# Kernel tuning notes

Measured on AMD Instinct MI355X. Metric: run time of the kernel, lower is better.

## Reference

```python
import jax, jax.numpy as jnp
import numpy as np

D_MODEL = 1024
N_HEADS = 16
D_FF = 4096
EPS = 1e-5


def setup_inputs() -> dict:
    key = jax.random.key(0)
    ks = jax.random.split(key, 10)
    sig_attn = (1.0 / D_MODEL) ** 0.5
    sig1 = (2.0 / (D_MODEL + D_FF)) ** 0.5
    sig2 = (2.0 / (D_FF + D_MODEL)) ** 0.5
    return {
        "x": jax.random.normal(ks[0], (4, 2048, D_MODEL), dtype=jnp.float32),
        "W_q": jax.random.normal(ks[1], (D_MODEL, D_MODEL), jnp.float32) * sig_attn,
        "W_k": jax.random.normal(ks[2], (D_MODEL, D_MODEL), jnp.float32) * sig_attn,
        "W_v": jax.random.normal(ks[3], (D_MODEL, D_MODEL), jnp.float32) * sig_attn,
        "W_o": jax.random.normal(ks[4], (D_MODEL, D_MODEL), jnp.float32) * sig_attn,
        "gamma1": jnp.ones((D_MODEL,), jnp.float32),
        "gamma2": jnp.ones((D_MODEL,), jnp.float32),
        "W1": jax.random.normal(ks[5], (D_FF, D_MODEL), jnp.float32) * sig1,  # gate proj
        "W2": jax.random.normal(ks[6], (D_MODEL, D_FF), jnp.float32) * sig2,  # down proj
        "W3": jax.random.normal(ks[7], (D_FF, D_MODEL), jnp.float32) * sig1,  # up proj
    }


def _rmsnorm(x, gamma, eps=EPS):
    # computed in fp32 as in the original, cast back to input dtype
    in_dtype = x.dtype
    xf = x.astype(jnp.float32)
    norm = jnp.sqrt(jnp.mean(xf * xf, axis=-1, keepdims=True) + eps)
    return ((xf / norm) * gamma).astype(in_dtype)


def _mha(x, W_q, W_k, W_v, W_o, n_heads=N_HEADS):
    B, S, D = x.shape
    d_h = D // n_heads
    # projections: weights stored as [d_out, d_in]
    q = jnp.einsum('bsd,ed->bse', x, W_q).reshape(B, S, n_heads, d_h).transpose(0, 2, 1, 3)
    k = jnp.einsum('bsd,ed->bse', x, W_k).reshape(B, S, n_heads, d_h).transpose(0, 2, 1, 3)
    v = jnp.einsum('bsd,ed->bse', x, W_v).reshape(B, S, n_heads, d_h).transpose(0, 2, 1, 3)
    scores = jnp.einsum('bhqd,bhkd->bhqk', q, k) / jnp.sqrt(jnp.asarray(d_h, x.dtype))
    causal = jnp.tril(jnp.ones((S, S), dtype=bool))  # True = keep
    scores = jnp.where(causal, scores, -jnp.inf)
    probs = jax.nn.softmax(scores, axis=-1)
    out = jnp.einsum('bhqk,bhkd->bhqd', probs, v)
    out = out.transpose(0, 2, 1, 3).reshape(B, S, D)
    return jnp.einsum('bse,de->bsd', out, W_o)


def _swiglu(x, W1, W2, W3):
    g = jnp.einsum('bsd,fd->bsf', x, W1)
    u = jnp.einsum('bsd,fd->bsf', x, W3)
    return jnp.einsum('bsf,df->bsd', jax.nn.silu(g) * u, W2)


def reference(x, W_q, W_k, W_v, W_o, gamma1, gamma2, W1, W2, W3):
    x = x + _mha(_rmsnorm(x, gamma1), W_q, W_k, W_v, W_o)
    x = x + _swiglu(_rmsnorm(x, gamma2), W1, W2, W3)
    return x
```

## Files before the change

kernel.cpp:

```cpp
#include <hip/hip_runtime.h>
#include <cstdint>
#include <cstddef>

typedef unsigned short u16;
typedef unsigned int u32;
typedef short bf16x8 __attribute__((ext_vector_type(8)));
typedef float f32x4 __attribute__((ext_vector_type(4)));
typedef float f32x16 __attribute__((ext_vector_type(16)));
typedef u16 u16x4 __attribute__((ext_vector_type(4)));

__device__ __forceinline__ u16 f2bf(float f) {
  u32 u = __float_as_uint(f);
  return (u16)((u + 0x7FFFu + ((u >> 16) & 1u)) >> 16);
}
__device__ __forceinline__ float bf2f(u16 h) {
  return __uint_as_float(((u32)h) << 16);
}
__device__ __forceinline__ u32 cvtpk(float lo, float hi) {
  u32 r;
  asm("v_cvt_pk_bf16_f32 %0, %1, %2" : "=v"(r) : "v"(lo), "v"(hi));
  return r;
}
__device__ __forceinline__ float exp2a(float x) {
  float r;
  asm("v_exp_f32 %0, %1" : "=v"(r) : "v"(x));
  return r;
}

__device__ __forceinline__ void gload_lds16(const void* g, void* l) {
  __builtin_amdgcn_global_load_lds((const __attribute__((address_space(1))) u32*)g,
                                   (__attribute__((address_space(3))) u32*)l, 16, 0, 0);
}

__global__ __launch_bounds__(256) void castw(const float* __restrict__ src,
                                             u16* __restrict__ dst, int n4) {
  int i = blockIdx.x * 256 + threadIdx.x;
  if (i < n4) {
    float4 v = ((const float4*)src)[i];
    u16x4 r;
    r.x = f2bf(v.x); r.y = f2bf(v.y); r.z = f2bf(v.z); r.w = f2bf(v.w);
    ((u16x4*)dst)[i] = r;
  }
}

__global__ __launch_bounds__(256) void rmsnorm_k(const float* __restrict__ x,
                                                 const float* __restrict__ gamma,
                                                 u16* __restrict__ o) {
  const int row = blockIdx.x;
  const int t = threadIdx.x;
  float4 v = ((const float4*)(x + (size_t)row * 1024))[t];
  float ss = v.x * v.x + v.y * v.y + v.z * v.z + v.w * v.w;
  #pragma unroll
  for (int m = 1; m < 64; m <<= 1) ss += __shfl_xor(ss, m);
  __shared__ float wsum[4];
  if ((t & 63) == 0) wsum[t >> 6] = ss;
  __syncthreads();
  float tot = wsum[0] + wsum[1] + wsum[2] + wsum[3];
  float inv = rsqrtf(tot * (1.0f / 1024.0f) + 1e-5f);
  float4 g = ((const float4*)gamma)[t];
  u16x4 r;
  r.x = f2bf(v.x * inv * g.x);
  r.y = f2bf(v.y * inv * g.y);
  r.z = f2bf(v.z * inv * g.z);
  r.w = f2bf(v.w * inv * g.w);
  ((u16x4*)(o + (size_t)row * 1024))[t] = r;
}

template <int EPI>
__global__ __launch_bounds__(256, 4)
void gemm128(const u16* __restrict__ A, const u16* __restrict__ B,
             void* out, const void* ep, int M, int N, int KLOOP, int KS,
             float scale, int ncut) {
  __shared__ u16 smem[2][8192];
  u16* const sA = smem[0];
  u16* const sB = smem[1];

  const int tid = threadIdx.x;
  const int lane = tid & 63;
  const int w = tid >> 6;
  const int wr = w >> 1, wc = w & 1;
  const int lr = lane & 15, lk = lane >> 4;

  A += (size_t)blockIdx.z * KLOOP;
  B += (size_t)blockIdx.z * KLOOP;

  const int nx = gridDim.x;
  const int nwg = nx * gridDim.y;
  const int flat = blockIdx.y * nx + blockIdx.x;
  const int qq = nwg >> 3, rr = nwg & 7;
  const int xcd = flat & 7, off = flat >> 3;
  const int swz = (xcd < rr ? xcd * (qq + 1) : rr * (qq + 1) + (xcd - rr) * qq) + off;
  const int sr = nx * 8;
  const int g8 = swz / sr, rem = swz % sr;
  const int m0 = (g8 * 8 + (rem & 7)) * 128;
  const int n0 = (rem >> 3) * 128;

  f32x4 acc[4][4];
  #pragma unroll
  for (int i = 0; i < 4; i++)
    #pragma unroll
    for (int j = 0; j < 4; j++) acc[i][j] = (f32x4){0.f, 0.f, 0.f, 0.f};

  for (int kt = 0; kt < KLOOP; kt += 64) {
    __syncthreads();
    #pragma unroll
    for (int r = 0; r < 4; r++) {
      const int q = r * 256 + tid;
      const int row = q >> 3;
      const int cs = (q & 7) ^ (row & 7);
      gload_lds16(A + (size_t)(m0 + row) * KS + kt + cs * 8, (char*)sA + q * 16);
      gload_lds16(B + (size_t)(n0 + row) * KS + kt + cs * 8, (char*)sB + q * 16);
    }
    __syncthreads();
    #pragma unroll
    for (int kk = 0; kk < 2; kk++) {
      bf16x8 a_[4], b_[4];
      #pragma unroll
      for (int i = 0; i < 4; i++)
        a_[i] = *(const bf16x8*)&sA[(wr * 64 + i * 16 + lr) * 64 +
                                    (((kk * 4 + lk) ^ (lr & 7)) * 8)];
      #pragma unroll
      for (int j = 0; j < 4; j++)
        b_[j] = *(const bf16x8*)&sB[(wc * 64 + j * 16 + lr) * 64 +
                                    (((kk * 4 + lk) ^ (lr & 7)) * 8)];
      #pragma unroll
      for (int i = 0; i < 4; i++)
        #pragma unroll
        for (int j = 0; j < 4; j++)
          acc[i][j] = __builtin_amdgcn_mfma_f32_16x16x32_bf16(a_[i], b_[j], acc[i][j], 0, 0, 0);
    }
  }

  if constexpr (EPI == 1 || EPI == 3) {
    #pragma unroll
    for (int i = 0; i < 4; i++)
      #pragma unroll
      for (int j = 0; j < 4; j++)
        #pragma unroll
        for (int r = 0; r < 4; r++) {
          const int grow = m0 + wr * 64 + i * 16 + lk * 4 + r;
          const int gcol = n0 + wc * 64 + j * 16 + lr;
          const size_t idx = (size_t)grow * N + gcol;
          if (EPI == 1) ((float*)out)[idx] = ((const float*)ep)[idx] + acc[i][j][r];
          else          unsafeAtomicAdd((float*)out + idx, acc[i][j][r]);
        }
  } else {
    u16* const smC = smem[0];
    const float s = (EPI == 0 && n0 < ncut) ? scale : 1.0f;
    __syncthreads();
    #pragma unroll
    for (int i = 0; i < 4; i++)
      #pragma unroll
      for (int j = 0; j < 4; j++)
        #pragma unroll
        for (int r = 0; r < 4; r++) {
          const int row = wr * 64 + i * 16 + lk * 4 + r;
          const int col = wc * 64 + j * 16 + lr;
          smC[row * 128 + (col ^ ((row & 7) << 3))] = f2bf(acc[i][j][r] * s);
        }
    __syncthreads();
    #pragma unroll
    for (int it = 0; it < 8; it++) {
      const int fl = it * 256 + tid;
      const int row = fl >> 4;
      const int ch = fl & 15;
      bf16x8 cv = *(const bf16x8*)&smC[row * 128 + ((ch ^ (row & 7)) * 8)];
      const size_t gidx = (size_t)(m0 + row) * N + n0 + ch * 8;
      if (EPI == 0) {
        *(bf16x8*)((u16*)out + gidx) = cv;
      } else {
        bf16x8 gv = *(const bf16x8*)((const u16*)ep + gidx);
        bf16x8 ov;
        #pragma unroll
        for (int k = 0; k < 8; k++) {
          float g = bf2f((u16)gv[k]);
          float sg = g / (1.f + __expf(-g));
          ov[k] = (short)f2bf(sg * bf2f((u16)cv[k]));
        }
        *(bf16x8*)((u16*)out + gidx) = ov;
      }
    }
  }
}

__global__ __launch_bounds__(256) void vtrans(const u16* __restrict__ qkv,
                                              u16* __restrict__ vt) {
  __shared__ u16 T[64][72];
  const int t = threadIdx.x;
  const int s0 = blockIdx.x * 64;
  const int h = blockIdx.y;
  const int b = blockIdx.z;
  const int sl = t >> 2, dl = (t & 3) * 16;
  const u16* src = qkv + ((size_t)(b * 2048 + s0 + sl)) * 3072 + 2048 + h * 64 + dl;
  bf16x8 v0 = *(const bf16x8*)src;
  bf16x8 v1 = *(const bf16x8*)(src + 8);
  #pragma unroll
  for (int j = 0; j < 8; j++) T[dl + j][sl] = (u16)v0[j];
  #pragma unroll
  for (int j = 0; j < 8; j++) T[dl + 8 + j][sl] = (u16)v1[j];
  __syncthreads();
  const int dl2 = t >> 2, sl2 = (t & 3) * 16;
  u16* dst = vt + ((size_t)((b * 16 + h) * 64 + dl2)) * 2048 + s0 + sl2;
  *(bf16x8*)dst = *(const bf16x8*)&T[dl2][sl2];
  *(bf16x8*)(dst + 8) = *(const bf16x8*)&T[dl2][sl2 + 8];
}

__global__ __launch_bounds__(256, 2)
void attn_fwd3(const u16* __restrict__ qkv, const u16* __restrict__ vt,
               u16* __restrict__ o) {
  __shared__ u16 sm[9216];
  u16* const smK = sm;
  u16* const smV = sm + 4096;

  const int tid = threadIdx.x;
  const int lane = tid & 63;
  const int w = tid >> 6;
  const int hi = lane >> 5;
  const int ln = lane & 31;

  const int bh = blockIdx.x;
  const int pair = blockIdx.y;
  const int b = bh >> 4, h = bh & 15;

  #pragma unroll 1
  for (int phase = 0; phase < 2; ++phase) {
    const int qt = phase ? (15 - pair) : pair;
    const int qbase = qt * 128;
    const int qw0 = qbase + w * 32;
    const int qglob = qw0 + ln;
    const int nkb = qt * 2 + 2;

    bf16x8 qf[4];
    {
      const u16* qp = qkv + ((size_t)(b * 2048 + qw0 + ln)) * 3072 + h * 64 + hi * 8;
      #pragma unroll
      for (int c = 0; c < 4; c++) qf[c] = *(const bf16x8*)(qp + c * 16);
    }

    f32x16 accO[2];
    #pragma unroll
    for (int i = 0; i < 2; i++)
      #pragma unroll
      for (int r = 0; r < 16; r++) accO[i][r] = 0.f;
    float mrun = -1e30f, lsum = 0.f;

    for (int kb = 0; kb < nkb; kb++) {
      const int kbase = kb * 64;
      __syncthreads();
      #pragma unroll
      for (int r = 0; r < 2; r++) {
        const int cb = w * 128 + r * 64;
        const int ci = cb + lane;
        {
          const int key = ci >> 3, gch = (ci & 7) ^ (key & 7);
          const u16* src = qkv + ((size_t)(b * 2048 + kbase + key)) * 3072 + 1024 + h * 64 + gch * 8;
          gload_lds16(src, (char*)smK + cb * 16);
        }
        {
          const int d = ci >> 3, gch = (ci & 7) ^ (d & 7);
          const u16* src = vt + ((size_t)(bh * 64 + d)) * 2048 + kbase + gch * 8;
          gload_lds16(src, (char*)smV + cb * 16);
        }
      }
      __syncthreads();

      if (kbase <= qw0 + 31) {
        f32x16 st[2];
        #pragma unroll
        for (int kt = 0; kt < 2; kt++) {
          #pragma unroll
          for (int r = 0; r < 16; r++) st[kt][r] = 0.f;
        }
        __builtin_amdgcn_s_setprio(1);
        #pragma unroll
        for (int kt = 0; kt < 2; kt++)
          #pragma unroll
          for (int c = 0; c < 4; c++) {
            const int row = kt * 32 + ln;
            const int sch = (c * 2 + hi) ^ (ln & 7);
            bf16x8 kf = *(const bf16x8*)((const char*)smK + row * 128 + sch * 16);
            st[kt] = __builtin_amdgcn_mfma_f32_32x32x16_bf16(kf, qf[c], st[kt], 0, 0, 0);
          }
        __builtin_amdgcn_s_setprio(0);
        if (kbase + 63 > qw0) {
          #pragma unroll
          for (int kt = 0; kt < 2; kt++)
            #pragma unroll
            for (int r = 0; r < 16; r++) {
              const int kk = kbase + kt * 32 + (r & 3) + 8 * (r >> 2) + 4 * hi;
              if (kk > qglob) st[kt][r] = -1e30f;
            }
        }
        float t16[16];
        #pragma unroll
        for (int i = 0; i < 16; i++) t16[i] = fmaxf(st[0][i], st[1][i]);
        #pragma unroll
        for (int s = 8; s > 0; s >>= 1)
          #pragma unroll
          for (int i = 0; i < 8; i++)
            if (i < s) t16[i] = fmaxf(t16[i], t16[i + s]);
        float pm = t16[0];
        pm = fmaxf(pm, __shfl_xor(pm, 32));
        if (!__all(pm - mrun <= 8.f)) {
          const float mnew = fmaxf(mrun, pm);
          const float alpha = exp2a(mrun - mnew);
          lsum *= alpha;
          accO[0] *= alpha;
          accO[1] *= alpha;
          mrun = mnew;
        }
        #pragma unroll
        for (int kt = 0; kt < 2; kt++)
          #pragma unroll
          for (int r = 0; r < 16; r++) st[kt][r] = exp2a(st[kt][r] - mrun);
        float s16[16];
        #pragma unroll
        for (int i = 0; i < 16; i++) s16[i] = st[0][i] + st[1][i];
        #pragma unroll
        for (int s = 8; s > 0; s >>= 1)
          #pragma unroll
          for (int i = 0; i < 8; i++)
            if (i < s) s16[i] = s16[i] + s16[i + s];
        float ps = s16[0];
        ps += __shfl_xor(ps, 32);
        lsum += ps;

        #pragma unroll
        for (int kt = 0; kt < 2; kt++) {
          u32 pw[8], px[8];
          #pragma unroll
          for (int i = 0; i < 8; i++) pw[i] = cvtpk(st[kt][2 * i], st[kt][2 * i + 1]);
          #pragma unroll
          for (int i = 0; i < 8; i++) px[i] = (u32)__shfl_xor((int)pw[i], 32);
          union { u32 wd[4]; bf16x8 v; } f0, f1;
          f0.wd[0] = hi ? px[2] : pw[0];
          f0.wd[1] = hi ? px[3] : pw[1];
          f0.wd[2] = hi ? pw[2] : px[0];
          f0.wd[3] = hi ? pw[3] : px[1];
          f1.wd[0] = hi ? px[6] : pw[4];
          f1.wd[1] = hi ? px[7] : pw[5];
          f1.wd[2] = hi ? pw[6] : px[4];
          f1.wd[3] = hi ? pw[7] : px[5];
          __builtin_amdgcn_s_setprio(1);
          #pragma unroll
          for (int d0 = 0; d0 < 2; d0++) {
            #pragma unroll
            for (int kc = 0; kc < 2; kc++) {
              const int drow = d0 * 32 + ln;
              const int sch = (kt * 4 + kc * 2 + hi) ^ (ln & 7);
              bf16x8 vf = *(const bf16x8*)((const char*)smV + drow * 128 + sch * 16);
              accO[d0] = __builtin_amdgcn_mfma_f32_32x32x16_bf16(vf, kc ? f1.v : f0.v,
                                                                 accO[d0], 0, 0, 0);
            }
          }
          __builtin_amdgcn_s_setprio(0);
        }
      }
    }

    __syncthreads();
    const float inv = 1.0f / lsum;
    #pragma unroll
    for (int d0 = 0; d0 < 2; d0++)
      #pragma unroll
      for (int r = 0; r < 16; r++) {
        const int d = d0 * 32 + (r & 3) + 8 * (r >> 2) + 4 * hi;
        sm[(w * 32 + ln) * 72 + d] = f2bf(accO[d0][r] * inv);
      }
    __syncthreads();
    const int ql = tid >> 1, dh = (tid & 1) * 32;
    const u16* srcp = &sm[ql * 72 + dh];
    u16* dst = o + ((size_t)(b * 2048 + qbase + ql)) * 1024 + h * 64 + dh;
    #pragma unroll
    for (int j = 0; j < 4; j++)
      *(bf16x8*)(dst + j * 8) = *(const bf16x8*)(srcp + j * 8);
    __syncthreads();
  }
}

extern "C" void kernel_launch(void* const* d_in, const int* in_sizes, int n_in,
                              void* d_out, int out_size, void* d_ws, size_t ws_size,
                              hipStream_t stream) {
  const float* x      = (const float*)d_in[0];
  const float* W_q    = (const float*)d_in[1];
  const float* W_k    = (const float*)d_in[2];
  const float* W_v    = (const float*)d_in[3];
  const float* W_o    = (const float*)d_in[4];
  const float* gamma1 = (const float*)d_in[5];
  const float* gamma2 = (const float*)d_in[6];
  const float* W1     = (const float*)d_in[7];
  const float* W2     = (const float*)d_in[8];
  const float* W3     = (const float*)d_in[9];

  char* ws = (char*)d_ws;
  const size_t MB = 1ull << 20;
  u16* qkvw  = (u16*)(ws + 0 * MB);
  u16* Wo_b  = (u16*)(ws + 6 * MB);
  u16* W1_b  = (u16*)(ws + 8 * MB);
  u16* W3_b  = (u16*)(ws + 16 * MB);
  u16* W2_b  = (u16*)(ws + 24 * MB);
  u16* xn    = (u16*)(ws + 32 * MB);
  u16* qkvb  = (u16*)(ws + 48 * MB);
  u16* attnb = (u16*)(ws + 96 * MB);
  u16* vtb   = (u16*)(ws + 112 * MB);
  u16* gbuf  = (u16*)(ws + 112 * MB);
  u16* hbuf  = (u16*)(ws + 48 * MB);
  float* x1  = (float*)d_out;

  castw<<<1024, 256, 0, stream>>>(W_q, qkvw, 262144);
  castw<<<1024, 256, 0, stream>>>(W_k, qkvw + 1024 * 1024, 262144);
  castw<<<1024, 256, 0, stream>>>(W_v, qkvw + 2048 * 1024, 262144);
  castw<<<1024, 256, 0, stream>>>(W_o, Wo_b, 262144);
  castw<<<4096, 256, 0, stream>>>(W1, W1_b, 1048576);
  castw<<<4096, 256, 0, stream>>>(W3, W3_b, 1048576);
  castw<<<4096, 256, 0, stream>>>(W2, W2_b, 1048576);

  rmsnorm_k<<<8192, 256, 0, stream>>>(x, gamma1, xn);
  gemm128<0><<<dim3(24, 64), 256, 0, stream>>>(xn, qkvw, qkvb, nullptr,
                                               8192, 3072, 1024, 1024,
                                               0.125f * 1.44269504f, 1024);
  vtrans<<<dim3(32, 16, 4), 256, 0, stream>>>(qkvb, vtb);
  attn_fwd3<<<dim3(64, 8), 256, 0, stream>>>(qkvb, vtb, attnb);
  gemm128<1><<<dim3(8, 64), 256, 0, stream>>>(attnb, Wo_b, x1, x,
                                              8192, 1024, 1024, 1024, 1.0f, 0);

  rmsnorm_k<<<8192, 256, 0, stream>>>(x1, gamma2, xn);
  gemm128<0><<<dim3(32, 64), 256, 0, stream>>>(xn, W1_b, gbuf, nullptr,
                                               8192, 4096, 1024, 1024, 1.0f, 0);
  gemm128<2><<<dim3(32, 64), 256, 0, stream>>>(xn, W3_b, hbuf, gbuf,
                                               8192, 4096, 1024, 1024, 1.0f, 0);
  gemm128<3><<<dim3(8, 64, 2), 256, 0, stream>>>(hbuf, W2_b, (float*)d_out, nullptr,
                                                 8192, 1024, 2048, 4096, 1.0f, 0);
}
```

Baseline: 489.5 us.

## Double-buffer LDS staging in attention and the W1 gate GEMM

Adds a double-buffered GEMM variant that prefetches the next K tile into a second LDS buffer while computing on the current one, with an XCD-aware workgroup swizzle. It is used only for the W1 gate projection. The attention kernel is also converted to double-buffered K/V staging, so each key block needs one barrier instead of two. The cost is twice the LDS per block, which is meant to hide global-to-LDS latency but lowers occupancy (launch bounds drop to 2 blocks per SM for the GEMM).

```diff
diff --git a/kernel.cpp b/kernel.cpp
--- a/kernel.cpp
+++ b/kernel.cpp
@@ -66,6 +66,7 @@
   ((u16x4*)(o + (size_t)row * 1024))[t] = r;
 }
 
+
 template <int EPI>
 __global__ __launch_bounds__(256, 4)
 void gemm128(const u16* __restrict__ A, const u16* __restrict__ B,
@@ -148,6 +149,131 @@
     u16* const smC = smem[0];
     const float s = (EPI == 0 && n0 < ncut) ? scale : 1.0f;
     __syncthreads();
+    #pragma unroll
+    for (int i = 0; i < 4; i++)
+      #pragma unroll
+      for (int j = 0; j < 4; j++)
+        #pragma unroll
+        for (int r = 0; r < 4; r++) {
+          const int row = wr * 64 + i * 16 + lk * 4 + r;
+          const int col = wc * 64 + j * 16 + lr;
+          smC[row * 128 + (col ^ ((row & 7) << 3))] = f2bf(acc[i][j][r] * s);
+        }
+    __syncthreads();
+    #pragma unroll
+    for (int it = 0; it < 8; it++) {
+      const int fl = it * 256 + tid;
+      const int row = fl >> 4;
+      const int ch = fl & 15;
+      bf16x8 cv = *(const bf16x8*)&smC[row * 128 + ((ch ^ (row & 7)) * 8)];
+      const size_t gidx = (size_t)(m0 + row) * N + n0 + ch * 8;
+      if (EPI == 0) {
+        *(bf16x8*)((u16*)out + gidx) = cv;
+      } else {
+        bf16x8 gv = *(const bf16x8*)((const u16*)ep + gidx);
+        bf16x8 ov;
+        #pragma unroll
+        for (int k = 0; k < 8; k++) {
+          float g = bf2f((u16)gv[k]);
+          float sg = g / (1.f + __expf(-g));
+          ov[k] = (short)f2bf(sg * bf2f((u16)cv[k]));
+        }
+        *(bf16x8*)((u16*)out + gidx) = ov;
+      }
+    }
+  }
+}
+
+template <int EPI>
+__global__ __launch_bounds__(256, 2)
+void gemm128db(const u16* __restrict__ A, const u16* __restrict__ B,
+               void* out, const void* ep, int M, int N, int KLOOP, int KS,
+               float scale, int ncut) {
+  __shared__ u16 sA[2][8192];
+  __shared__ u16 sB[2][8192];
+
+  const int tid = threadIdx.x;
+  const int lane = tid & 63;
+  const int w = tid >> 6;
+  const int wr = w >> 1, wc = w & 1;
+  const int lr = lane & 15, lk = lane >> 4;
+
+  A += (size_t)blockIdx.z * KLOOP;
+  B += (size_t)blockIdx.z * KLOOP;
+
+  const int nx = gridDim.x;
+  const int nwg = nx * gridDim.y;
+  const int flat = blockIdx.y * nx + blockIdx.x;
+  const int qq = nwg >> 3, rr = nwg & 7;
+  const int xcd = flat & 7, off = flat >> 3;
+  const int swz = (xcd < rr ? xcd * (qq + 1) : rr * (qq + 1) + (xcd - rr) * qq) + off;
+  const int sr = nx * 8;
+  const int g8 = swz / sr, rem = swz % sr;
+  const int m0 = (g8 * 8 + (rem & 7)) * 128;
+  const int n0 = (rem >> 3) * 128;
+
+  f32x4 acc[4][4];
+  #pragma unroll
+  for (int i = 0; i < 4; i++)
+    #pragma unroll
+    for (int j = 0; j < 4; j++) acc[i][j] = (f32x4){0.f, 0.f, 0.f, 0.f};
+
+  #define STAGE128(BUF, KT)                                                       \
+    _Pragma("unroll")                                                             \
+    for (int r = 0; r < 4; r++) {                                                 \
+      const int q = r * 256 + tid;                                                \
+      const int row = q >> 3;                                                     \
+      const int cs = (q & 7) ^ (row & 7);                                         \
+      gload_lds16(A + (size_t)(m0 + row) * KS + (KT) + cs * 8,                    \
+                  (char*)sA[BUF] + q * 16);                                       \
+      gload_lds16(B + (size_t)(n0 + row) * KS + (KT) + cs * 8,                    \
+                  (char*)sB[BUF] + q * 16);                                       \
+    }
+
+  const int NT = KLOOP >> 6;
+  STAGE128(0, 0)
+  __syncthreads();
+
+  for (int W = 0; W < NT; ++W) {
+    const int buf = W & 1;
+    if (W + 1 < NT) { STAGE128(buf ^ 1, (W + 1) << 6) }
+    #pragma unroll
+    for (int kk = 0; kk < 2; kk++) {
+      bf16x8 a_[4], b_[4];
+      #pragma unroll
+      for (int i = 0; i < 4; i++)
+        a_[i] = *(const bf16x8*)&sA[buf][(wr * 64 + i * 16 + lr) * 64 +
+                                        (((kk * 4 + lk) ^ (lr & 7)) * 8)];
+      #pragma unroll
+      for (int j = 0; j < 4; j++)
+        b_[j] = *(const bf16x8*)&sB[buf][(wc * 64 + j * 16 + lr) * 64 +
+                                         (((kk * 4 + lk) ^ (lr & 7)) * 8)];
+      #pragma unroll
+      for (int i = 0; i < 4; i++)
+        #pragma unroll
+        for (int j = 0; j < 4; j++)
+          acc[i][j] = __builtin_amdgcn_mfma_f32_16x16x32_bf16(a_[i], b_[j], acc[i][j], 0, 0, 0);
+    }
+    __syncthreads();
+  }
+  #undef STAGE128
+
+  if constexpr (EPI == 1 || EPI == 3) {
+    #pragma unroll
+    for (int i = 0; i < 4; i++)
+      #pragma unroll
+      for (int j = 0; j < 4; j++)
+        #pragma unroll
+        for (int r = 0; r < 4; r++) {
+          const int grow = m0 + wr * 64 + i * 16 + lk * 4 + r;
+          const int gcol = n0 + wc * 64 + j * 16 + lr;
+          const size_t idx = (size_t)grow * N + gcol;
+          if (EPI == 1) ((float*)out)[idx] = ((const float*)ep)[idx] + acc[i][j][r];
+          else          unsafeAtomicAdd((float*)out + idx, acc[i][j][r]);
+        }
+  } else {
+    u16* const smC = sA[0];
+    const float s = (EPI == 0 && n0 < ncut) ? scale : 1.0f;
     #pragma unroll
     for (int i = 0; i < 4; i++)
       #pragma unroll
@@ -206,12 +332,9 @@
 }
 
 __global__ __launch_bounds__(256, 2)
-void attn_fwd3(const u16* __restrict__ qkv, const u16* __restrict__ vt,
+void attn_fwd4(const u16* __restrict__ qkv, const u16* __restrict__ vt,
                u16* __restrict__ o) {
-  __shared__ u16 sm[9216];
-  u16* const smK = sm;
-  u16* const smV = sm + 4096;
-
+  __shared__ u16 sm[16384];
   const int tid = threadIdx.x;
   const int lane = tid & 63;
   const int w = tid >> 6;
@@ -221,6 +344,24 @@
   const int bh = blockIdx.x;
   const int pair = blockIdx.y;
   const int b = bh >> 4, h = bh & 15;
+
+  #define ATTN_STAGE(BUF, KB)                                                         \
+    _Pragma("unroll")                                                                 \
+    for (int r = 0; r < 2; r++) {                                                     \
+      const int cb = w * 128 + r * 64;                                                \
+      const int ci = cb + lane;                                                       \
+      {                                                                               \
+        const int key = ci >> 3, gch = (ci & 7) ^ (key & 7);                          \
+        const u16* src = qkv + ((size_t)(b * 2048 + (KB) * 64 + key)) * 3072 + 1024 + \
+                         h * 64 + gch * 8;                                            \
+        gload_lds16(src, (char*)(sm + (BUF) * 4096) + cb * 16);                       \
+      }                                                                               \
+      {                                                                               \
+        const int d = ci >> 3, gch = (ci & 7) ^ (d & 7);                              \
+        const u16* src = vt + ((size_t)(bh * 64 + d)) * 2048 + (KB) * 64 + gch * 8;   \
+        gload_lds16(src, (char*)(sm + 8192 + (BUF) * 4096) + cb * 16);                \
+      }                                                                               \
+    }
 
   #pragma unroll 1
   for (int phase = 0; phase < 2; ++phase) {
@@ -244,25 +385,15 @@
       for (int r = 0; r < 16; r++) accO[i][r] = 0.f;
     float mrun = -1e30f, lsum = 0.f;
 
+    ATTN_STAGE(0, 0)
+    __syncthreads();
+
     for (int kb = 0; kb < nkb; kb++) {
       const int kbase = kb * 64;
-      __syncthreads();
-      #pragma unroll
-      for (int r = 0; r < 2; r++) {
-        const int cb = w * 128 + r * 64;
-        const int ci = cb + lane;
-        {
-          const int key = ci >> 3, gch = (ci & 7) ^ (key & 7);
-          const u16* src = qkv + ((size_t)(b * 2048 + kbase + key)) * 3072 + 1024 + h * 64 + gch * 8;
-          gload_lds16(src, (char*)smK + cb * 16);
-        }
-        {
-          const int d = ci >> 3, gch = (ci & 7) ^ (d & 7);
-          const u16* src = vt + ((size_t)(bh * 64 + d)) * 2048 + kbase + gch * 8;
-          gload_lds16(src, (char*)smV + cb * 16);
-        }
-      }
-      __syncthreads();
+      const int buf = kb & 1;
+      if (kb + 1 < nkb) { ATTN_STAGE(buf ^ 1, kb + 1) }
+      const u16* smK = sm + buf * 4096;
+      const u16* smV = sm + 8192 + buf * 4096;
 
       if (kbase <= qw0 + 31) {
         f32x16 st[2];
@@ -356,9 +487,9 @@
           __builtin_amdgcn_s_setprio(0);
         }
       }
-    }
-
-    __syncthreads();
+      __syncthreads();
+    }
+
     const float inv = 1.0f / lsum;
     #pragma unroll
     for (int d0 = 0; d0 < 2; d0++)
@@ -376,6 +507,7 @@
       *(bf16x8*)(dst + j * 8) = *(const bf16x8*)(srcp + j * 8);
     __syncthreads();
   }
+  #undef ATTN_STAGE
 }
 
 extern "C" void kernel_launch(void* const* d_in, const int* in_sizes, int n_in,
@@ -420,13 +552,13 @@
                                                8192, 3072, 1024, 1024,
                                                0.125f * 1.44269504f, 1024);
   vtrans<<<dim3(32, 16, 4), 256, 0, stream>>>(qkvb, vtb);
-  attn_fwd3<<<dim3(64, 8), 256, 0, stream>>>(qkvb, vtb, attnb);
+  attn_fwd4<<<dim3(64, 8), 256, 0, stream>>>(qkvb, vtb, attnb);
   gemm128<1><<<dim3(8, 64), 256, 0, stream>>>(attnb, Wo_b, x1, x,
                                               8192, 1024, 1024, 1024, 1.0f, 0);
 
   rmsnorm_k<<<8192, 256, 0, stream>>>(x1, gamma2, xn);
-  gemm128<0><<<dim3(32, 64), 256, 0, stream>>>(xn, W1_b, gbuf, nullptr,
-                                               8192, 4096, 1024, 1024, 1.0f, 0);
+  gemm128db<0><<<dim3(32, 64), 256, 0, stream>>>(xn, W1_b, gbuf, nullptr,
+                                                 8192, 4096, 1024, 1024, 1.0f, 0);
   gemm128<2><<<dim3(32, 64), 256, 0, stream>>>(xn, W3_b, hbuf, gbuf,
                                                8192, 4096, 1024, 1024, 1.0f, 0);
   gemm128<3><<<dim3(8, 64, 2), 256, 0, stream>>>(hbuf, W2_b, (float*)d_out, nullptr,
```

Measured after the change: 510.3 us. 4.2% more time.

## Fuse gate and up projections into one GEMM with interleaved weights

Applied to the files above, without the earlier changes.

Packs W1 and W3 into one interleaved bf16 weight matrix, with 64-row blocks alternating gate and up, so each 128-wide output tile holds matching gate and up columns. A single GEMM with a new SwiGLU epilogue then computes silu(g)*u directly from shared memory. This removes the separate gate GEMM launch, the write of the gate intermediate to global memory and its read-back in the second GEMM. The SwiGLU output is written at half width into a new buffer offset.

```diff
diff --git a/kernel.cpp b/kernel.cpp
--- a/kernel.cpp
+++ b/kernel.cpp
@@ -41,6 +41,18 @@
     r.x = f2bf(v.x); r.y = f2bf(v.y); r.z = f2bf(v.z); r.w = f2bf(v.w);
     ((u16x4*)dst)[i] = r;
   }
+}
+
+__global__ __launch_bounds__(256) void castw_pack(const float* __restrict__ src,
+                                                  u16* __restrict__ dst, int half) {
+  int i = blockIdx.x * 256 + threadIdx.x;
+  float4 v = ((const float4*)src)[i];
+  const int n = i >> 8;
+  const int c4 = i & 255;
+  const int orow = ((n >> 6) << 7) + (half << 6) + (n & 63);
+  u16x4 r;
+  r.x = f2bf(v.x); r.y = f2bf(v.y); r.z = f2bf(v.z); r.w = f2bf(v.w);
+  ((u16x4*)dst)[orow * 256 + c4] = r;
 }
 
 __global__ __launch_bounds__(256) void rmsnorm_k(const float* __restrict__ x,
@@ -159,25 +171,33 @@
           smC[row * 128 + (col ^ ((row & 7) << 3))] = f2bf(acc[i][j][r] * s);
         }
     __syncthreads();
-    #pragma unroll
-    for (int it = 0; it < 8; it++) {
-      const int fl = it * 256 + tid;
-      const int row = fl >> 4;
-      const int ch = fl & 15;
-      bf16x8 cv = *(const bf16x8*)&smC[row * 128 + ((ch ^ (row & 7)) * 8)];
-      const size_t gidx = (size_t)(m0 + row) * N + n0 + ch * 8;
-      if (EPI == 0) {
+    if constexpr (EPI == 4) {
+      #pragma unroll
+      for (int it = 0; it < 4; it++) {
+        const int fl = it * 256 + tid;
+        const int row = fl >> 3;
+        const int ch = fl & 7;
+        bf16x8 gvv = *(const bf16x8*)&smC[row * 128 + ((ch ^ (row & 7)) * 8)];
+        bf16x8 uvv = *(const bf16x8*)&smC[row * 128 + (((ch + 8) ^ (row & 7)) * 8)];
+        bf16x8 ov;
+        #pragma unroll
+        for (int k = 0; k < 8; k++) {
+          float g = bf2f((u16)gvv[k]);
+          float u = bf2f((u16)uvv[k]);
+          float sg = g / (1.f + __expf(-g));
+          ov[k] = (short)f2bf(sg * u);
+        }
+        *(bf16x8*)((u16*)out + (size_t)(m0 + row) * N + (n0 >> 1) + ch * 8) = ov;
+      }
+    } else {
+      #pragma unroll
+      for (int it = 0; it < 8; it++) {
+        const int fl = it * 256 + tid;
+        const int row = fl >> 4;
+        const int ch = fl & 15;
+        bf16x8 cv = *(const bf16x8*)&smC[row * 128 + ((ch ^ (row & 7)) * 8)];
+        const size_t gidx = (size_t)(m0 + row) * N + n0 + ch * 8;
         *(bf16x8*)((u16*)out + gidx) = cv;
-      } else {
-        bf16x8 gv = *(const bf16x8*)((const u16*)ep + gidx);
-        bf16x8 ov;
-        #pragma unroll
-        for (int k = 0; k < 8; k++) {
-          float g = bf2f((u16)gv[k]);
-          float sg = g / (1.f + __expf(-g));
-          ov[k] = (short)f2bf(sg * bf2f((u16)cv[k]));
-        }
-        *(bf16x8*)((u16*)out + gidx) = ov;
       }
     }
   }
@@ -396,23 +416,21 @@
   const size_t MB = 1ull << 20;
   u16* qkvw  = (u16*)(ws + 0 * MB);
   u16* Wo_b  = (u16*)(ws + 6 * MB);
-  u16* W1_b  = (u16*)(ws + 8 * MB);
-  u16* W3_b  = (u16*)(ws + 16 * MB);
+  u16* W13   = (u16*)(ws + 8 * MB);
   u16* W2_b  = (u16*)(ws + 24 * MB);
   u16* xn    = (u16*)(ws + 32 * MB);
   u16* qkvb  = (u16*)(ws + 48 * MB);
   u16* attnb = (u16*)(ws + 96 * MB);
   u16* vtb   = (u16*)(ws + 112 * MB);
-  u16* gbuf  = (u16*)(ws + 112 * MB);
-  u16* hbuf  = (u16*)(ws + 48 * MB);
+  u16* hbuf  = (u16*)(ws + 128 * MB);
   float* x1  = (float*)d_out;
 
   castw<<<1024, 256, 0, stream>>>(W_q, qkvw, 262144);
   castw<<<1024, 256, 0, stream>>>(W_k, qkvw + 1024 * 1024, 262144);
   castw<<<1024, 256, 0, stream>>>(W_v, qkvw + 2048 * 1024, 262144);
   castw<<<1024, 256, 0, stream>>>(W_o, Wo_b, 262144);
-  castw<<<4096, 256, 0, stream>>>(W1, W1_b, 1048576);
-  castw<<<4096, 256, 0, stream>>>(W3, W3_b, 1048576);
+  castw_pack<<<4096, 256, 0, stream>>>(W1, W13, 0);
+  castw_pack<<<4096, 256, 0, stream>>>(W3, W13, 1);
   castw<<<4096, 256, 0, stream>>>(W2, W2_b, 1048576);
 
   rmsnorm_k<<<8192, 256, 0, stream>>>(x, gamma1, xn);
@@ -425,9 +443,7 @@
                                               8192, 1024, 1024, 1024, 1.0f, 0);
 
   rmsnorm_k<<<8192, 256, 0, stream>>>(x1, gamma2, xn);
-  gemm128<0><<<dim3(32, 64), 256, 0, stream>>>(xn, W1_b, gbuf, nullptr,
-                                               8192, 4096, 1024, 1024, 1.0f, 0);
-  gemm128<2><<<dim3(32, 64), 256, 0, stream>>>(xn, W3_b, hbuf, gbuf,
+  gemm128<4><<<dim3(64, 64), 256, 0, stream>>>(xn, W13, hbuf, nullptr,
                                                8192, 4096, 1024, 1024, 1.0f, 0);
   gemm128<3><<<dim3(8, 64, 2), 256, 0, stream>>>(hbuf, W2_b, (float*)d_out, nullptr,
                                                  8192, 1024, 2048, 4096, 1.0f, 0);
```

New measurement: 475.9 us. -2.8%, faster.
